# Kernel tuning notes

Measured on AMD Instinct MI355X. Metric: run time of the kernel, lower is better.

## Reference

```python
import jax, jax.numpy as jnp
import numpy as np
import math

B, T, C = 4, 2048, 1024
H, D = 16, 64  # n_head, head_dim; H*D == C

def setup_inputs() -> dict:
    key = jax.random.key(0)
    ks = jax.random.split(key, 8)
    s = 1.0 / math.sqrt(C)
    return {
        "x": jax.random.normal(ks[0], (B, T, C), jnp.float32),
        "W_attn": jax.random.normal(ks[1], (C, 3 * C), jnp.float32) * s,
        "b_attn": jax.random.normal(ks[2], (3 * C,), jnp.float32) * 0.02,
        "W_proj": jax.random.normal(ks[3], (C, C), jnp.float32) * s,
        "b_proj": jax.random.normal(ks[4], (C,), jnp.float32) * 0.02,
        "bQ": jax.random.normal(ks[5], (H, D), jnp.float32) * 0.02,
        "bK": jax.random.normal(ks[6], (H, D), jnp.float32) * 0.02,
        "bV": jax.random.normal(ks[7], (H, D), jnp.float32) * 0.02,
    }

def reference(x, W_attn, b_attn, W_proj, b_proj, bQ, bK, bV):
    Bx, Tx, Cx = x.shape
    qkv = x @ W_attn + b_attn                       # [B,T,3C]
    q, k, v = jnp.split(qkv, 3, axis=-1)
    def heads(t):
        return t.reshape(Bx, Tx, H, D).transpose(0, 2, 1, 3)  # [B,H,T,D]
    q = heads(q) + bQ[None, :, None, :]
    k = heads(k) + bK[None, :, None, :]
    v = heads(v) + bV[None, :, None, :]
    scale = 1.0 / math.sqrt(D)
    scores = jnp.einsum('bhqd,bhkd->bhqk', q, k) * scale      # [B,H,T,T]
    causal = jnp.tril(jnp.ones((Tx, Tx), dtype=bool))
    scores = jnp.where(causal[None, None], scores, -jnp.inf)
    att = jax.nn.softmax(scores, axis=-1)
    y = jnp.einsum('bhqk,bhkd->bhqd', att, v)                 # [B,H,T,D]
    y = y.transpose(0, 2, 1, 3).reshape(Bx, Tx, Cx)
    return y @ W_proj + b_proj
```

## Files before the change

### kernel.cpp

```cpp
#include <hip/hip_runtime.h>
#include <hip/hip_bf16.h>

#define BB 4
#define TT 2048
#define CC 1024
#define HH 16
#define DD 64

typedef __bf16 bf16x8 __attribute__((ext_vector_type(8)));
typedef float f32x4 __attribute__((ext_vector_type(4)));
typedef unsigned int u32x4 __attribute__((ext_vector_type(4)));
typedef unsigned int u32x2 __attribute__((ext_vector_type(2)));
typedef unsigned short u16x8 __attribute__((ext_vector_type(8)));
typedef unsigned short u16x4 __attribute__((ext_vector_type(4)));
typedef unsigned int u32;

__device__ __forceinline__ unsigned short f2bf(float f) {
  u32 u = __builtin_bit_cast(u32, f);
  u += 0x7fff + ((u >> 16) & 1);
  return (unsigned short)(u >> 16);
}

__device__ __forceinline__ float exp2_raw(float x) {
  float r;
  asm("v_exp_f32 %0, %1" : "=v"(r) : "v"(x));
  return r;
}

__device__ __forceinline__ bf16x8 lds_load8(const unsigned short* p) {
  u32x4 t = *(const u32x4*)p;
  return __builtin_bit_cast(bf16x8, t);
}

__device__ __forceinline__ void g2l16(const unsigned short* g, unsigned short* l) {
  __builtin_amdgcn_global_load_lds(
      (const __attribute__((address_space(1))) u32*)g,
      (__attribute__((address_space(3))) u32*)l, 16, 0, 0);
}

__global__ __launch_bounds__(256) void prep(
    const float* __restrict__ x, const float* __restrict__ Wa,
    const float* __restrict__ Wp, unsigned short* __restrict__ xb,
    unsigned short* __restrict__ Wta, unsigned short* __restrict__ Wtp)
{
  __shared__ unsigned short T[64 * 68];
  const int tid = threadIdx.x;
  const int bid = blockIdx.x;
  if (bid < 4096) {
    int i = (bid * 256 + tid) * 8;
    f32x4 a = *(const f32x4*)(x + i);
    f32x4 b = *(const f32x4*)(x + i + 4);
    u16x8 o;
    o[0] = f2bf(a[0]); o[1] = f2bf(a[1]); o[2] = f2bf(a[2]); o[3] = f2bf(a[3]);
    o[4] = f2bf(b[0]); o[5] = f2bf(b[1]); o[6] = f2bf(b[2]); o[7] = f2bf(b[3]);
    *(u16x8*)(xb + i) = o;
    return;
  }
  const float* W; unsigned short* Wt; int N, n0, k0;
  if (bid < 4096 + 768) {
    int b2 = bid - 4096;  W = Wa; Wt = Wta; N = 3072;
    n0 = (b2 % 48) * 64;  k0 = (b2 / 48) * 64;
  } else {
    int b2 = bid - 4864;  W = Wp; Wt = Wtp; N = 1024;
    n0 = (b2 % 16) * 64;  k0 = (b2 / 16) * 64;
  }
#pragma unroll
  for (int it = 0; it < 4; ++it) {
    int idx = it * 256 + tid;
    int kk = idx >> 4, nn = (idx & 15) * 4;
    f32x4 v = *(const f32x4*)(W + (size_t)(k0 + kk) * N + n0 + nn);
    u16x4 p;
    p[0] = f2bf(v[0]); p[1] = f2bf(v[1]); p[2] = f2bf(v[2]); p[3] = f2bf(v[3]);
    *(u16x4*)(&T[kk * 68 + nn]) = p;
  }
  __syncthreads();
#pragma unroll
  for (int it = 0; it < 4; ++it) {
    int idx = it * 256 + tid;
    int nn = idx >> 4, kc = (idx & 15) * 4;
    u16x4 o;
    o[0] = T[(kc + 0) * 68 + nn];
    o[1] = T[(kc + 1) * 68 + nn];
    o[2] = T[(kc + 2) * 68 + nn];
    o[3] = T[(kc + 3) * 68 + nn];
    *(u16x4*)(Wt + (size_t)(n0 + nn) * 1024 + k0 + kc) = o;
  }
}

__global__ __launch_bounds__(256) void qkv_gemm(
    const unsigned short* __restrict__ xb, const unsigned short* __restrict__ Wt,
    const float* __restrict__ b_attn, const float* __restrict__ bQ,
    const float* __restrict__ bK, const float* __restrict__ bV,
    unsigned short* __restrict__ Qb, unsigned short* __restrict__ Kb,
    unsigned short* __restrict__ Vb)
{
  __shared__ unsigned short S[16384];
  const int tid = threadIdx.x;
  const int w = tid >> 6, lane = tid & 63;
  const int l16 = lane & 15, quad = lane >> 4;
  const int xcd = blockIdx.x & 7, kk = blockIdx.x >> 3;
  const int mblk = xcd * 8 + (kk & 7), nblk = kk >> 3;
  const int m0 = mblk * 128, n0 = nblk * 128;
  const int wm = (w & 1) * 64, wn = (w >> 1) * 64;

  const int srow = lane >> 3;
  const int schunk = ((lane & 7) ^ (srow & 7)) * 8;
  const unsigned short* ga = xb + (size_t)(m0 + w * 8 + srow) * 1024 + schunk;
  const unsigned short* gb = Wt + (size_t)(n0 + w * 8 + srow) * 1024 + schunk;
  unsigned short* la = &S[(w * 8) * 64];
  unsigned short* lb = &S[8192 + (w * 8) * 64];

  f32x4 acc[4][4] = {};

  for (int kb = 0; kb < 1024; kb += 64) {
    __syncthreads();
#pragma unroll
    for (int i = 0; i < 4; ++i) {
      g2l16(ga + kb + (size_t)i * 32 * 1024, la + i * 32 * 64);
      g2l16(gb + kb + (size_t)i * 32 * 1024, lb + i * 32 * 64);
    }
    __syncthreads();
    bf16x8 af[4][2], bfr[4][2];
#pragma unroll
    for (int mi = 0; mi < 4; ++mi)
#pragma unroll
      for (int dk = 0; dk < 2; ++dk)
        af[mi][dk] = lds_load8(
            &S[(wm + mi * 16 + l16) * 64 + (((dk * 4 + quad) ^ (l16 & 7)) * 8)]);
#pragma unroll
    for (int ni = 0; ni < 4; ++ni)
#pragma unroll
      for (int dk = 0; dk < 2; ++dk)
        bfr[ni][dk] = lds_load8(
            &S[8192 + (wn + ni * 16 + l16) * 64 + (((dk * 4 + quad) ^ (l16 & 7)) * 8)]);
#pragma unroll
    for (int mi = 0; mi < 4; ++mi)
#pragma unroll
      for (int ni = 0; ni < 4; ++ni) {
        acc[mi][ni] = __builtin_amdgcn_mfma_f32_16x16x32_bf16(
            af[mi][0], bfr[ni][0], acc[mi][ni], 0, 0, 0);
        acc[mi][ni] = __builtin_amdgcn_mfma_f32_16x16x32_bf16(
            af[mi][1], bfr[ni][1], acc[mi][ni], 0, 0, 0);
      }
  }

  if (nblk >= 16) {
    float biasv[4];
    unsigned short* dst[4];
#pragma unroll
    for (int ni = 0; ni < 4; ++ni) {
      int col = n0 + wn + ni * 16 + l16;
      int cc = col & 1023;
      biasv[ni] = b_attn[col] + bV[cc];
      dst[ni] = Vb + (size_t)(cc >> 6) * (DD * TT) + (size_t)(cc & 63) * TT;
    }
#pragma unroll
    for (int mi = 0; mi < 4; ++mi) {
      const int mbase = m0 + wm + mi * 16 + quad * 4;
      int bidx = mbase >> 11, t = mbase & 2047;
      size_t co = (size_t)bidx * (HH * TT * DD);
#pragma unroll
      for (int ni = 0; ni < 4; ++ni) {
        u16x4 pkt;
#pragma unroll
        for (int r = 0; r < 4; ++r)
          pkt[r] = f2bf(acc[mi][ni][r] + biasv[ni]);
        *(u16x4*)(dst[ni] + co + t) = pkt;
      }
    }
  } else {
    const float scq = (nblk < 8) ? 0.125f * 1.44269504f : 1.0f;
    unsigned short* gbase = (nblk < 8) ? Qb : Kb;
    const float* hb = (nblk < 8) ? bQ : bK;
    float biasv[4];
#pragma unroll
    for (int ni = 0; ni < 4; ++ni) {
      int col = n0 + wn + ni * 16 + l16;
      biasv[ni] = b_attn[col] + hb[col & 1023];
    }
#pragma unroll
    for (int p = 0; p < 2; ++p) {
      __syncthreads();
      if ((w & 1) == p) {
#pragma unroll
        for (int mi = 0; mi < 4; ++mi)
#pragma unroll
          for (int ni = 0; ni < 4; ++ni)
#pragma unroll
            for (int r = 0; r < 4; ++r) {
              int row = mi * 16 + quad * 4 + r;
              int col = wn + ni * 16 + l16;
              S[row * 136 + col] = f2bf((acc[mi][ni][r] + biasv[ni]) * scq);
            }
      }
      __syncthreads();
#pragma unroll
      for (int i = 0; i < 8; ++i) {
        int fid = i * 256 + tid;
        int row = fid >> 5, col0 = (fid & 31) * 4;
        u16x4 v = *(const u16x4*)&S[row * 136 + col0];
        int cc0 = (n0 + col0) & 1023;
        int m = m0 + p * 64 + row;
        int bidx = m >> 11, t = m & 2047;
        *(u16x4*)(gbase + (size_t)bidx * (HH * TT * DD)
                  + (size_t)(cc0 >> 6) * (TT * DD) + (size_t)t * 64 + (cc0 & 63)) = v;
      }
    }
  }
}

__global__ __launch_bounds__(256) void attn_kernel(
    const unsigned short* __restrict__ Qb, const unsigned short* __restrict__ Kb,
    const unsigned short* __restrict__ Vtg, unsigned short* __restrict__ Yb)
{
  __shared__ unsigned short Kl[2 * 4096];
  __shared__ unsigned short Vl[2 * 4096];
  __shared__ unsigned short Pl[4 * 32 * 72];
  const int tid = threadIdx.x;
  const int w = tid >> 6, lane = tid & 63;
  const int l16 = lane & 15, quad = lane >> 4;
  const int qt = 15 - (blockIdx.x >> 6);
  const int bh = blockIdx.x & 63;
  const int b = bh >> 4, h = bh & 15;
  const int q0 = qt * 128, qw = q0 + w * 32;

  const unsigned short* Qg = Qb + (size_t)bh * TT * DD;
  const unsigned short* Kg = Kb + (size_t)bh * TT * DD;
  const unsigned short* Vg = Vtg + (size_t)bh * DD * TT;

  bf16x8 qf[2][2];
#pragma unroll
  for (int mi = 0; mi < 2; ++mi)
#pragma unroll
    for (int dk = 0; dk < 2; ++dk) {
      u32x4 t = *(const u32x4*)(Qg + (size_t)(qw + mi * 16 + l16) * 64 + dk * 32 + quad * 8);
      qf[mi][dk] = __builtin_bit_cast(bf16x8, t);
    }

  f32x4 accO[2][4] = {};
  f32x4 accL[2] = {};
  u16x8 o16;
#pragma unroll
  for (int j = 0; j < 8; ++j) o16[j] = 0x3F80;
  const bf16x8 onesf = __builtin_bit_cast(bf16x8, o16);

  const int srow = w * 8 + (lane >> 3);
  const int schunk = ((lane & 7) ^ (srow & 7)) * 8;
  const int kkey = 4 * (srow & 15) + (srow >> 4);
  const unsigned short* gk1 = Kg + (size_t)kkey * 64 + schunk;
  const unsigned short* gk2 = Kg + (size_t)(kkey + 2) * 64 + schunk;
  const unsigned short* gv1 = Vg + (size_t)srow * TT + schunk;
  const unsigned short* gv2 = Vg + (size_t)(srow + 32) * TT + schunk;

  const int kend = q0 + 64;

  g2l16(gk1, &Kl[w * 512]);
  g2l16(gk2, &Kl[w * 512 + 2048]);
  g2l16(gv1, &Vl[w * 512]);
  g2l16(gv2, &Vl[w * 512 + 2048]);
  __syncthreads();

  int cur = 0;
  for (int k0 = 0; k0 <= kend; k0 += 64) {
    const int nxt = (cur ^ 1) * 4096;
    if (k0 + 64 <= kend) {
      g2l16(gk1 + (size_t)(k0 + 64) * 64, &Kl[nxt + w * 512]);
      g2l16(gk2 + (size_t)(k0 + 64) * 64, &Kl[nxt + w * 512 + 2048]);
      g2l16(gv1 + (k0 + 64), &Vl[nxt + w * 512]);
      g2l16(gv2 + (k0 + 64), &Vl[nxt + w * 512 + 2048]);
    }
    if (k0 <= qw + 31) {
      const int co = cur * 4096;

      f32x4 accS[2][4] = {};
      __builtin_amdgcn_s_setprio(1);
#pragma unroll
      for (int ni = 0; ni < 4; ++ni)
#pragma unroll
        for (int dk = 0; dk < 2; ++dk) {
          bf16x8 kf = lds_load8(
              &Kl[co + (ni * 16 + l16) * 64 + (((dk * 4 + quad) ^ (l16 & 7)) * 8)]);
#pragma unroll
          for (int mi = 0; mi < 2; ++mi)
            accS[mi][ni] = __builtin_amdgcn_mfma_f32_16x16x32_bf16(
                qf[mi][dk], kf, accS[mi][ni], 0, 0, 0);
        }
      __builtin_amdgcn_s_setprio(0);

      const bool maskT = (k0 + 63 > qw);
#pragma unroll
      for (int mi = 0; mi < 2; ++mi)
#pragma unroll
        for (int r = 0; r < 4; ++r) {
          int qrow = qw + mi * 16 + quad * 4 + r;
          float s0 = accS[mi][0][r], s1 = accS[mi][1][r];
          float s2 = accS[mi][2][r], s3 = accS[mi][3][r];
          if (maskT) {
            int kb = k0 + 4 * l16;
            if (kb + 0 > qrow) s0 = -3e38f;
            if (kb + 1 > qrow) s1 = -3e38f;
            if (kb + 2 > qrow) s2 = -3e38f;
            if (kb + 3 > qrow) s3 = -3e38f;
          }
          u32 e0 = __builtin_bit_cast(u32, exp2_raw(s0));
          u32 e1 = __builtin_bit_cast(u32, exp2_raw(s1));
          u32 e2 = __builtin_bit_cast(u32, exp2_raw(s2));
          u32 e3 = __builtin_bit_cast(u32, exp2_raw(s3));
          u32x2 pv;
          pv[0] = __builtin_amdgcn_perm(e1, e0, 0x07060302);
          pv[1] = __builtin_amdgcn_perm(e3, e2, 0x07060302);
          *(u32x2*)(&Pl[(w * 32 + mi * 16 + quad * 4 + r) * 72 + 4 * l16]) = pv;
        }

      __builtin_amdgcn_s_setprio(1);
#pragma unroll
      for (int kc = 0; kc < 2; ++kc) {
        bf16x8 pf[2];
#pragma unroll
        for (int mi = 0; mi < 2; ++mi)
          pf[mi] = lds_load8(&Pl[(w * 32 + mi * 16 + l16) * 72 + kc * 32 + quad * 8]);
#pragma unroll
        for (int dn = 0; dn < 4; ++dn) {
          bf16x8 vf = lds_load8(
              &Vl[co + (dn * 16 + l16) * 64 + (((kc * 4 + quad) ^ (l16 & 7)) * 8)]);
#pragma unroll
          for (int mi = 0; mi < 2; ++mi)
            accO[mi][dn] = __builtin_amdgcn_mfma_f32_16x16x32_bf16(
                pf[mi], vf, accO[mi][dn], 0, 0, 0);
        }
#pragma unroll
        for (int mi = 0; mi < 2; ++mi)
          accL[mi] = __builtin_amdgcn_mfma_f32_16x16x32_bf16(
              pf[mi], onesf, accL[mi], 0, 0, 0);
      }
      __builtin_amdgcn_s_setprio(0);
    }
    __syncthreads();
    cur ^= 1;
  }

#pragma unroll
  for (int mi = 0; mi < 2; ++mi)
#pragma unroll
    for (int r = 0; r < 4; ++r) {
      int q = qw + mi * 16 + quad * 4 + r;
      float inv = 1.0f / accL[mi][r];
      size_t base = ((size_t)b * TT + q) * CC + h * DD;
#pragma unroll
      for (int dn = 0; dn < 4; ++dn)
        Yb[base + dn * 16 + l16] = f2bf(accO[mi][dn][r] * inv);
    }
}

__global__ __launch_bounds__(256) void proj_gemm(
    const unsigned short* __restrict__ Yb, const unsigned short* __restrict__ Wt,
    const float* __restrict__ bp, float* __restrict__ out)
{
  __shared__ unsigned short Al[128 * 64];
  __shared__ unsigned short Bl[128 * 64];
  const int tid = threadIdx.x;
  const int w = tid >> 6, lane = tid & 63;
  const int l16 = lane & 15, quad = lane >> 4;
  const int xcd = blockIdx.x & 7, kk = blockIdx.x >> 3;
  const int mblk = xcd * 8 + (kk & 7), nblk = kk >> 3;
  const int m0 = mblk * 128, n0 = nblk * 128;
  const int wm = (w & 1) * 64, wn = (w >> 1) * 64;

  const int srow = lane >> 3;
  const int schunk = ((lane & 7) ^ (srow & 7)) * 8;
  const unsigned short* ga = Yb + (size_t)(m0 + w * 8 + srow) * 1024 + schunk;
  const unsigned short* gb = Wt + (size_t)(n0 + w * 8 + srow) * 1024 + schunk;
  unsigned short* la = &Al[(w * 8) * 64];
  unsigned short* lb = &Bl[(w * 8) * 64];

  f32x4 acc[4][4] = {};

  for (int kb = 0; kb < 1024; kb += 64) {
    __syncthreads();
#pragma unroll
    for (int i = 0; i < 4; ++i) {
      g2l16(ga + kb + (size_t)i * 32 * 1024, la + i * 32 * 64);
      g2l16(gb + kb + (size_t)i * 32 * 1024, lb + i * 32 * 64);
    }
    __syncthreads();
    bf16x8 af[4][2], bfr[4][2];
#pragma unroll
    for (int mi = 0; mi < 4; ++mi)
#pragma unroll
      for (int dk = 0; dk < 2; ++dk)
        af[mi][dk] = lds_load8(
            &Al[(wm + mi * 16 + l16) * 64 + (((dk * 4 + quad) ^ (l16 & 7)) * 8)]);
#pragma unroll
    for (int ni = 0; ni < 4; ++ni)
#pragma unroll
      for (int dk = 0; dk < 2; ++dk)
        bfr[ni][dk] = lds_load8(
            &Bl[(wn + ni * 16 + l16) * 64 + (((dk * 4 + quad) ^ (l16 & 7)) * 8)]);
#pragma unroll
    for (int mi = 0; mi < 4; ++mi)
#pragma unroll
      for (int ni = 0; ni < 4; ++ni) {
        acc[mi][ni] = __builtin_amdgcn_mfma_f32_16x16x32_bf16(
            af[mi][0], bfr[ni][0], acc[mi][ni], 0, 0, 0);
        acc[mi][ni] = __builtin_amdgcn_mfma_f32_16x16x32_bf16(
            af[mi][1], bfr[ni][1], acc[mi][ni], 0, 0, 0);
      }
  }

#pragma unroll
  for (int mi = 0; mi < 4; ++mi)
#pragma unroll
    for (int r = 0; r < 4; ++r) {
      int m = m0 + wm + mi * 16 + quad * 4 + r;
#pragma unroll
      for (int ni = 0; ni < 4; ++ni) {
        int c = n0 + wn + ni * 16 + l16;
        out[(size_t)m * 1024 + c] = acc[mi][ni][r] + bp[c];
      }
    }
}

extern "C" void kernel_launch(void* const* d_in, const int* in_sizes, int n_in,
                              void* d_out, int out_size, void* d_ws, size_t ws_size,
                              hipStream_t stream) {
  const float* x      = (const float*)d_in[0];
  const float* W_attn = (const float*)d_in[1];
  const float* b_attn = (const float*)d_in[2];
  const float* W_proj = (const float*)d_in[3];
  const float* b_proj = (const float*)d_in[4];
  const float* bQ     = (const float*)d_in[5];
  const float* bK     = (const float*)d_in[6];
  const float* bV     = (const float*)d_in[7];
  float* out = (float*)d_out;

  unsigned short* xb   = (unsigned short*)d_ws;
  unsigned short* Yb   = xb;
  unsigned short* Wt_a = xb + 8388608;
  unsigned short* Wt_p = Wt_a + 3145728;
  unsigned short* Qb   = Wt_p + 1048576;
  unsigned short* Kb   = Qb + 8388608;
  unsigned short* Vb   = Kb + 8388608;

  prep<<<dim3(4096 + 768 + 256), dim3(256), 0, stream>>>(x, W_attn, W_proj,
                                                         xb, Wt_a, Wt_p);
  qkv_gemm<<<dim3(64 * 24), dim3(256), 0, stream>>>(xb, Wt_a, b_attn, bQ, bK, bV,
                                                    Qb, Kb, Vb);
  attn_kernel<<<dim3(16 * 64), dim3(256), 0, stream>>>(Qb, Kb, Vb, Yb);
  proj_gemm<<<dim3(64 * 8), dim3(256), 0, stream>>>(Yb, Wt_p, b_proj, out);
}
```

Measured before the change: 247.5 us.

## Compute transposed scores to keep P in registers and skip LDS round-trip

Swaps the MFMA operand order so the score tile is produced transposed (keys along rows held per lane), which lets each lane pack its exp'd probabilities directly into the bf16x8 B-operand of the PV MFMA instead of writing P to shared memory and reloading it. The K tile load permutation is changed so that the permuted key order matches the register layout. The output store is also vectorized to 4-element packed writes. It removes the Pl LDS buffer and its store/load traffic, at the cost of a more intricate key permutation that must stay consistent with the masking index math.

```diff
diff --git a/kernel.cpp b/kernel.cpp
--- a/kernel.cpp
+++ b/kernel.cpp
@@ -215,7 +215,6 @@
 {
   __shared__ unsigned short Kl[2 * 4096];
   __shared__ unsigned short Vl[2 * 4096];
-  __shared__ unsigned short Pl[4 * 32 * 72];
   const int tid = threadIdx.x;
   const int w = tid >> 6, lane = tid & 63;
   const int l16 = lane & 15, quad = lane >> 4;
@@ -238,7 +237,7 @@
     }
 
   f32x4 accO[2][4] = {};
-  f32x4 accL[2] = {};
+  f32x4 accLt[2] = {};
   u16x8 o16;
 #pragma unroll
   for (int j = 0; j < 8; ++j) o16[j] = 0x3F80;
@@ -246,9 +245,9 @@
 
   const int srow = w * 8 + (lane >> 3);
   const int schunk = ((lane & 7) ^ (srow & 7)) * 8;
-  const int kkey = 4 * (srow & 15) + (srow >> 4);
+  const int kkey = 8 * ((srow >> 2) & 3) + 4 * ((srow >> 4) & 1) + (srow & 3);
   const unsigned short* gk1 = Kg + (size_t)kkey * 64 + schunk;
-  const unsigned short* gk2 = Kg + (size_t)(kkey + 2) * 64 + schunk;
+  const unsigned short* gk2 = Kg + (size_t)(kkey + 32) * 64 + schunk;
   const unsigned short* gv1 = Vg + (size_t)srow * TT + schunk;
   const unsigned short* gv2 = Vg + (size_t)(srow + 32) * TT + schunk;
 
@@ -283,42 +282,46 @@
 #pragma unroll
           for (int mi = 0; mi < 2; ++mi)
             accS[mi][ni] = __builtin_amdgcn_mfma_f32_16x16x32_bf16(
-                qf[mi][dk], kf, accS[mi][ni], 0, 0, 0);
+                kf, qf[mi][dk], accS[mi][ni], 0, 0, 0);
         }
       __builtin_amdgcn_s_setprio(0);
 
       const bool maskT = (k0 + 63 > qw);
-#pragma unroll
-      for (int mi = 0; mi < 2; ++mi)
-#pragma unroll
-        for (int r = 0; r < 4; ++r) {
-          int qrow = qw + mi * 16 + quad * 4 + r;
-          float s0 = accS[mi][0][r], s1 = accS[mi][1][r];
-          float s2 = accS[mi][2][r], s3 = accS[mi][3][r];
+      u32 pb[2][2][4];
+#pragma unroll
+      for (int mi = 0; mi < 2; ++mi) {
+        const int q = qw + mi * 16 + l16;
+#pragma unroll
+        for (int ni = 0; ni < 4; ++ni) {
+          float s0 = accS[mi][ni][0], s1 = accS[mi][ni][1];
+          float s2 = accS[mi][ni][2], s3 = accS[mi][ni][3];
           if (maskT) {
-            int kb = k0 + 4 * l16;
-            if (kb + 0 > qrow) s0 = -3e38f;
-            if (kb + 1 > qrow) s1 = -3e38f;
-            if (kb + 2 > qrow) s2 = -3e38f;
-            if (kb + 3 > qrow) s3 = -3e38f;
+            const int kb = k0 + 32 * (ni >> 1) + 8 * quad + 4 * (ni & 1);
+            if (kb + 0 > q) s0 = -3e38f;
+            if (kb + 1 > q) s1 = -3e38f;
+            if (kb + 2 > q) s2 = -3e38f;
+            if (kb + 3 > q) s3 = -3e38f;
           }
           u32 e0 = __builtin_bit_cast(u32, exp2_raw(s0));
           u32 e1 = __builtin_bit_cast(u32, exp2_raw(s1));
           u32 e2 = __builtin_bit_cast(u32, exp2_raw(s2));
           u32 e3 = __builtin_bit_cast(u32, exp2_raw(s3));
-          u32x2 pv;
-          pv[0] = __builtin_amdgcn_perm(e1, e0, 0x07060302);
-          pv[1] = __builtin_amdgcn_perm(e3, e2, 0x07060302);
-          *(u32x2*)(&Pl[(w * 32 + mi * 16 + quad * 4 + r) * 72 + 4 * l16]) = pv;
+          pb[mi][ni >> 1][2 * (ni & 1) + 0] = __builtin_amdgcn_perm(e1, e0, 0x07060302);
+          pb[mi][ni >> 1][2 * (ni & 1) + 1] = __builtin_amdgcn_perm(e3, e2, 0x07060302);
         }
+      }
 
       __builtin_amdgcn_s_setprio(1);
 #pragma unroll
       for (int kc = 0; kc < 2; ++kc) {
         bf16x8 pf[2];
 #pragma unroll
-        for (int mi = 0; mi < 2; ++mi)
-          pf[mi] = lds_load8(&Pl[(w * 32 + mi * 16 + l16) * 72 + kc * 32 + quad * 8]);
+        for (int mi = 0; mi < 2; ++mi) {
+          u32x4 t;
+          t[0] = pb[mi][kc][0]; t[1] = pb[mi][kc][1];
+          t[2] = pb[mi][kc][2]; t[3] = pb[mi][kc][3];
+          pf[mi] = __builtin_bit_cast(bf16x8, t);
+        }
 #pragma unroll
         for (int dn = 0; dn < 4; ++dn) {
           bf16x8 vf = lds_load8(
@@ -326,12 +329,12 @@
 #pragma unroll
           for (int mi = 0; mi < 2; ++mi)
             accO[mi][dn] = __builtin_amdgcn_mfma_f32_16x16x32_bf16(
-                pf[mi], vf, accO[mi][dn], 0, 0, 0);
+                vf, pf[mi], accO[mi][dn], 0, 0, 0);
         }
 #pragma unroll
         for (int mi = 0; mi < 2; ++mi)
-          accL[mi] = __builtin_amdgcn_mfma_f32_16x16x32_bf16(
-              pf[mi], onesf, accL[mi], 0, 0, 0);
+          accLt[mi] = __builtin_amdgcn_mfma_f32_16x16x32_bf16(
+              onesf, pf[mi], accLt[mi], 0, 0, 0);
       }
       __builtin_amdgcn_s_setprio(0);
     }
@@ -340,16 +343,19 @@
   }
 
 #pragma unroll
-  for (int mi = 0; mi < 2; ++mi)
-#pragma unroll
-    for (int r = 0; r < 4; ++r) {
-      int q = qw + mi * 16 + quad * 4 + r;
-      float inv = 1.0f / accL[mi][r];
-      size_t base = ((size_t)b * TT + q) * CC + h * DD;
-#pragma unroll
-      for (int dn = 0; dn < 4; ++dn)
-        Yb[base + dn * 16 + l16] = f2bf(accO[mi][dn][r] * inv);
-    }
+  for (int mi = 0; mi < 2; ++mi) {
+    const int q = qw + mi * 16 + l16;
+    const float inv = 1.0f / accLt[mi][0];
+    size_t base = ((size_t)b * TT + q) * CC + h * DD + quad * 4;
+#pragma unroll
+    for (int dn = 0; dn < 4; ++dn) {
+      u16x4 pkt;
+#pragma unroll
+      for (int rr = 0; rr < 4; ++rr)
+        pkt[rr] = f2bf(accO[mi][dn][rr] * inv);
+      *(u16x4*)(Yb + base + dn * 16) = pkt;
+    }
+  }
 }
 
 __global__ __launch_bounds__(256) void proj_gemm(
```

New measurement: 240.8 us. -2.7%, faster.
